# Performance work log

Measured on AMD Instinct MI355X. Metric: run time of the kernel, lower is better.

The kernel has to match this reference:

```python
import jax, jax.numpy as jnp
import numpy as np

D, H, KVH, HD, FF = 768, 12, 4, 64, 2048
N_REP = H // KVH
EPS = 1e-6


def rmsnorm(x, w):
    # Faithful to source: norm = ||x|| * n^{-1/2}; eps added to norm (not inside sqrt)
    norm = jnp.sqrt(jnp.sum(x * x, axis=-1, keepdims=True)) * (x.shape[-1] ** -0.5)
    return w * x / (norm + EPS)


def rope_tables(seq_len, head_dim, base=10000.0):
    inv_freq = 1.0 / (base ** (np.arange(0, head_dim, 2, dtype=np.float32) / head_dim))
    t = np.arange(seq_len, dtype=np.float32)
    freqs = np.einsum('i,j->ij', t, inv_freq)  # [S, HD/2]
    emb = np.concatenate([freqs, freqs], axis=-1)  # [S, HD]
    return jnp.asarray(np.cos(emb)), jnp.asarray(np.sin(emb))


def rotate_half(x):
    h = x.shape[-1] // 2
    return jnp.concatenate([-x[..., h:], x[..., :h]], axis=-1)


def setup_inputs() -> dict:
    key = jax.random.key(0)
    ks = jax.random.split(key, 9)
    s = 0.02
    return {
        'x': jax.random.normal(ks[0], (2, 2048, D), jnp.float32),
        'Wq': jax.random.normal(ks[1], (H * HD, D), jnp.float32) * s,
        'Wk': jax.random.normal(ks[2], (KVH * HD, D), jnp.float32) * s,
        'Wv': jax.random.normal(ks[3], (KVH * HD, D), jnp.float32) * s,
        'Wo': jax.random.normal(ks[4], (D, H * HD), jnp.float32) * s,
        'Wgate': jax.random.normal(ks[5], (FF, D), jnp.float32) * s,
        'Wup': jax.random.normal(ks[6], (FF, D), jnp.float32) * s,
        'Wdown': jax.random.normal(ks[7], (D, FF), jnp.float32) * s,
        'g1': jnp.ones((D,), jnp.float32),
        'g2': jnp.ones((D,), jnp.float32),
    }


def reference(x, Wq, Wk, Wv, Wo, Wgate, Wup, Wdown, g1, g2):
    B, S, _ = x.shape
    # ---- attention sublayer (pre-norm) ----
    xn = rmsnorm(x, g1)
    q = (xn @ Wq.T).reshape(B, S, H, HD).transpose(0, 2, 1, 3)      # [B,H,S,HD]
    k = (xn @ Wk.T).reshape(B, S, KVH, HD).transpose(0, 2, 1, 3)    # [B,KVH,S,HD]
    v = (xn @ Wv.T).reshape(B, S, KVH, HD).transpose(0, 2, 1, 3)
    cos, sin = rope_tables(S, HD)                                   # [S,HD]
    q = q * cos + rotate_half(q) * sin
    k = k * cos + rotate_half(k) * sin
    # repeat kv heads to match q heads
    k = jnp.repeat(k, N_REP, axis=1)                                # [B,H,S,HD]
    v = jnp.repeat(v, N_REP, axis=1)
    scores = jnp.einsum('bhqd,bhkd->bhqk', q, k) / jnp.sqrt(jnp.float32(HD))
    causal = jnp.tril(jnp.ones((S, S), bool))
    scores = jnp.where(causal, scores, jnp.finfo(scores.dtype).min)
    attn = jax.nn.softmax(scores, axis=-1)
    out = jnp.einsum('bhqk,bhkd->bhqd', attn, v)                    # [B,H,S,HD]
    out = out.transpose(0, 2, 1, 3).reshape(B, S, H * HD) @ Wo.T
    x = x + out
    # ---- SwiGLU FFN sublayer (pre-norm) ----
    xn2 = rmsnorm(x, g2)
    ff = (jax.nn.silu(xn2 @ Wgate.T) * (xn2 @ Wup.T)) @ Wdown.T
    return x + ff
```

## Files before the change

### kernel.cpp

```cpp
#include <hip/hip_runtime.h>
#include <hip/hip_bf16.h>
#include <math.h>

typedef __bf16 bf16;
typedef __attribute__((ext_vector_type(8))) __bf16 bf16x8;
typedef __attribute__((ext_vector_type(4))) __bf16 bf16x4;
typedef __attribute__((ext_vector_type(4))) float f32x4;

#define MFMA16(a,b,c) __builtin_amdgcn_mfma_f32_16x16x32_bf16(a,b,c,0,0,0)

#define BATCH 2
#define SEQ   2048
#define DMODEL 768
#define NH    12
#define NKV   4
#define NREP  3
#define HD    64
#define FFDIM 2048
#define ROWS  (BATCH*SEQ)

#define QSCALE 0.18033688011112042f
#define LOG2E  1.4426950408889634f

#define WB(N) asm volatile("s_waitcnt vmcnt(" #N ")\n\ts_barrier" ::: "memory")
#define BAR() asm volatile("s_barrier" ::: "memory")

__device__ __forceinline__ void gl2lds16(const bf16* g, bf16* l) {
  __builtin_amdgcn_global_load_lds(
      (const __attribute__((address_space(1))) void*)g,
      (__attribute__((address_space(3))) void*)l, 16, 0, 0);
}

struct Cvt7 { const float* s[7]; bf16* d[7]; int n[7]; };
__global__ __launch_bounds__(256) void cvt_all_kernel(Cvt7 c) {
  int seg = blockIdx.y;
  const float* __restrict__ src = c.s[seg];
  bf16* __restrict__ dst = c.d[seg];
  int n = c.n[seg];
  int stride = gridDim.x * 256;
  for (int i = blockIdx.x * 256 + threadIdx.x; i < n; i += stride)
    dst[i] = (bf16)src[i];
}

__global__ __launch_bounds__(256) void rope_tab_kernel(float* __restrict__ tab) {
  int id = blockIdx.x * 256 + threadIdx.x;
  int j = id >> 11, s = id & 2047;
  float inv = expf(-(float)j * (9.210340371976184f / 32.0f));
  float ang = (float)s * inv;
  tab[id] = cosf(ang);
  tab[65536 + id] = sinf(ang);
}

__global__ __launch_bounds__(192) void rmsnorm_kernel(const float* __restrict__ x,
    const float* __restrict__ g, bf16* __restrict__ out) {
  int row = blockIdx.x;
  const float* xr = x + (size_t)row * DMODEL;
  int t = threadIdx.x;
  f32x4 v = *(const f32x4*)(xr + t * 4);
  float ss = v[0] * v[0] + v[1] * v[1] + v[2] * v[2] + v[3] * v[3];
  #pragma unroll
  for (int off = 32; off; off >>= 1) ss += __shfl_xor(ss, off, 64);
  __shared__ float red[3];
  if ((t & 63) == 0) red[t >> 6] = ss;
  __syncthreads();
  float total = red[0] + red[1] + red[2];
  float norm = sqrtf(total) * 0.03608439182435161f;
  float sc = 1.0f / (norm + 1e-6f);
  f32x4 gv = *(const f32x4*)(g + t * 4);
  bf16x4 o;
  #pragma unroll
  for (int i = 0; i < 4; ++i) o[i] = (bf16)(gv[i] * v[i] * sc);
  *(bf16x4*)(out + (size_t)row * DMODEL + t * 4) = o;
}

__global__ __launch_bounds__(256) void gemm_pipe64_kernel(const bf16* __restrict__ A,
    const bf16* __restrict__ B, float* __restrict__ C, const float* __restrict__ R,
    int N, int K) {
  __shared__ __align__(16) bf16 At[4][64 * 32];
  __shared__ __align__(16) bf16 Bt[4][64 * 32];
  int t = threadIdx.x, lane = t & 63, wave = t >> 6;
  int l15 = lane & 15, lq = lane >> 4;
  int wrow = (wave >> 1) * 32, wcol = (wave & 1) * 32;
  int row0 = blockIdx.y * 64, col0 = blockIdx.x * 64;
  const bf16* Ag = A + (size_t)(row0 + (t >> 2)) * K + (t & 3) * 8;
  const bf16* Bg = B + (size_t)(col0 + (t >> 2)) * K + (t & 3) * 8;
  const int NS = K / 32;

  #pragma unroll
  for (int s = 0; s < 4; ++s) {
    int ks = s * 32;
    gl2lds16(Ag + ks, At[s] + t * 8);
    gl2lds16(Bg + ks, Bt[s] + t * 8);
  }

  f32x4 zero = {0.f, 0.f, 0.f, 0.f};
  f32x4 acc[2][2];
  #pragma unroll
  for (int m = 0; m < 2; ++m)
    #pragma unroll
    for (int n = 0; n < 2; ++n) acc[m][n] = zero;

  #define GP_COMPUTE(slot) do {                                              \
    const bf16* at = At[slot]; const bf16* bt = Bt[slot];                    \
    bf16x8 af[2], bfr[2];                                                    \
    _Pragma("unroll")                                                        \
    for (int m = 0; m < 2; ++m)                                              \
      af[m] = *(const bf16x8*)(at + (wrow + m * 16 + l15) * 32 + lq * 8);    \
    _Pragma("unroll")                                                        \
    for (int n = 0; n < 2; ++n)                                              \
      bfr[n] = *(const bf16x8*)(bt + (wcol + n * 16 + l15) * 32 + lq * 8);   \
    _Pragma("unroll")                                                        \
    for (int m = 0; m < 2; ++m)                                              \
      _Pragma("unroll")                                                      \
      for (int n = 0; n < 2; ++n)                                            \
        acc[m][n] = MFMA16(af[m], bfr[n], acc[m][n]);                        \
  } while (0)

  for (int k = 0; k < NS - 3; ++k) {
    WB(6);
    GP_COMPUTE(k & 3);
    BAR();
    if (k <= NS - 5) {
      int ks = (k + 4) * 32;
      gl2lds16(Ag + ks, At[k & 3] + t * 8);
      gl2lds16(Bg + ks, Bt[k & 3] + t * 8);
    }
  }
  for (int k = NS - 3; k < NS; ++k) {
    WB(0);
    GP_COMPUTE(k & 3);
  }
  #undef GP_COMPUTE

  #pragma unroll
  for (int m = 0; m < 2; ++m)
    #pragma unroll
    for (int n = 0; n < 2; ++n)
      #pragma unroll
      for (int r = 0; r < 4; ++r) {
        size_t idx = (size_t)(row0 + wrow + m * 16 + lq * 4 + r) * N
                   + (col0 + wcol + n * 16 + l15);
        C[idx] = acc[m][n][r] + R[idx];
      }
}

__global__ __launch_bounds__(256) void gemm_qkv_kernel(const bf16* __restrict__ A,
    const bf16* __restrict__ Wcat, const float* __restrict__ tab,
    bf16* __restrict__ Qh, bf16* __restrict__ Kh, bf16* __restrict__ Vt) {
  __shared__ __align__(16) bf16 At[4][64 * 32];
  __shared__ __align__(16) bf16 Bt[4][128 * 32];
  const int K = DMODEL;
  int t = threadIdx.x, lane = t & 63, wave = t >> 6;
  int l15 = lane & 15, lq = lane >> 4;
  int wrow = (wave >> 1) * 32, wcol = (wave & 1) * 64;
  int row0 = blockIdx.y * 64, col0 = blockIdx.x * 128;
  const bf16* Ag  = A + (size_t)(row0 + (t >> 2)) * K + (t & 3) * 8;
  const bf16* Bg0 = Wcat + (size_t)(col0 + (t >> 2)) * K + (t & 3) * 8;
  const bf16* Bg1 = Bg0 + (size_t)64 * K;
  const int NS = K / 32;

  #pragma unroll
  for (int s = 0; s < 4; ++s) {
    int ks = s * 32;
    gl2lds16(Ag + ks,  At[s] + t * 8);
    gl2lds16(Bg0 + ks, Bt[s] + t * 8);
    gl2lds16(Bg1 + ks, Bt[s] + 2048 + t * 8);
  }

  f32x4 zero = {0.f, 0.f, 0.f, 0.f};
  f32x4 acc[2][4];
  #pragma unroll
  for (int m = 0; m < 2; ++m)
    #pragma unroll
    for (int n = 0; n < 4; ++n) acc[m][n] = zero;

  #define QK_COMPUTE(slot) do {                                              \
    const bf16* at = At[slot]; const bf16* bt = Bt[slot];                    \
    bf16x8 af[2], bfr[4];                                                    \
    _Pragma("unroll")                                                        \
    for (int m = 0; m < 2; ++m)                                              \
      af[m] = *(const bf16x8*)(at + (wrow + m * 16 + l15) * 32 + lq * 8);    \
    _Pragma("unroll")                                                        \
    for (int n = 0; n < 4; ++n)                                              \
      bfr[n] = *(const bf16x8*)(bt + (wcol + n * 16 + l15) * 32 + lq * 8);   \
    _Pragma("unroll")                                                        \
    for (int m = 0; m < 2; ++m)                                              \
      _Pragma("unroll")                                                      \
      for (int n = 0; n < 4; ++n)                                            \
        acc[m][n] = MFMA16(af[m], bfr[n], acc[m][n]);                        \
  } while (0)

  for (int k = 0; k < NS - 3; ++k) {
    WB(9);
    QK_COMPUTE(k & 3);
    BAR();
    if (k <= NS - 5) {
      int ks = (k + 4) * 32;
      gl2lds16(Ag + ks,  At[k & 3] + t * 8);
      gl2lds16(Bg0 + ks, Bt[k & 3] + t * 8);
      gl2lds16(Bg1 + ks, Bt[k & 3] + 2048 + t * 8);
    }
  }
  for (int k = NS - 3; k < NS; ++k) {
    WB(0);
    QK_COMPUTE(k & 3);
  }
  #undef QK_COMPUTE

  int b = row0 >> 11;
  int s0 = (row0 & 2047) + wrow + lq * 4;
  int colw = col0 + wcol;
  if (colw < 768) {
    int h = colw >> 6;
    f32x4 cv[2][2], sv[2][2];
    #pragma unroll
    for (int m = 0; m < 2; ++m)
      #pragma unroll
      for (int jh = 0; jh < 2; ++jh) {
        const float* cp = tab + (jh * 16 + l15) * 2048 + s0 + m * 16;
        cv[m][jh] = *(const f32x4*)cp;
        sv[m][jh] = *(const f32x4*)(cp + 65536);
      }
    #pragma unroll
    for (int m = 0; m < 2; ++m)
      #pragma unroll
      for (int n = 0; n < 4; ++n) {
        float sgn = (n < 2) ? -1.f : 1.f;
        #pragma unroll
        for (int r = 0; r < 4; ++r) {
          float c = cv[m][n & 1][r], si = sv[m][n & 1][r];
          float rp = (acc[m][n][r] * c + sgn * acc[m][n ^ 2][r] * si) * QSCALE;
          Qh[((size_t)(b * NH + h) * SEQ + s0 + m * 16 + r) * 64 + n * 16 + l15] = (bf16)rp;
        }
      }
  } else if (colw < 1024) {
    int kh = (colw - 768) >> 6;
    f32x4 cv[2][2], sv[2][2];
    #pragma unroll
    for (int m = 0; m < 2; ++m)
      #pragma unroll
      for (int jh = 0; jh < 2; ++jh) {
        const float* cp = tab + (jh * 16 + l15) * 2048 + s0 + m * 16;
        cv[m][jh] = *(const f32x4*)cp;
        sv[m][jh] = *(const f32x4*)(cp + 65536);
      }
    #pragma unroll
    for (int m = 0; m < 2; ++m)
      #pragma unroll
      for (int n = 0; n < 4; ++n) {
        float sgn = (n < 2) ? -1.f : 1.f;
        #pragma unroll
        for (int r = 0; r < 4; ++r) {
          float c = cv[m][n & 1][r], si = sv[m][n & 1][r];
          float rp = acc[m][n][r] * c + sgn * acc[m][n ^ 2][r] * si;
          Kh[((size_t)(b * NKV + kh) * SEQ + s0 + m * 16 + r) * 64 + n * 16 + l15] = (bf16)rp;
        }
      }
  } else {
    int vh = (colw - 1024) >> 6;
    #pragma unroll
    for (int m = 0; m < 2; ++m)
      #pragma unroll
      for (int n = 0; n < 4; ++n) {
        bf16x4 pv;
        #pragma unroll
        for (int r = 0; r < 4; ++r) pv[r] = (bf16)acc[m][n][r];
        *(bf16x4*)(Vt + ((size_t)(b * NKV + vh) * 64 + n * 16 + l15) * SEQ + s0 + m * 16) = pv;
      }
  }
}

__global__ __launch_bounds__(256) void gemm_gu_kernel(const bf16* __restrict__ A,
    const bf16* __restrict__ Wg, const bf16* __restrict__ Wu, bf16* __restrict__ H) {
  __shared__ __align__(16) bf16 At[3][128 * 32];
  __shared__ __align__(16) bf16 Bgt[3][64 * 32];
  __shared__ __align__(16) bf16 But[3][64 * 32];
  const int K = DMODEL;
  int t = threadIdx.x, lane = t & 63, wave = t >> 6;
  int l15 = lane & 15, lq = lane >> 4;
  int wrow = (wave >> 1) * 64, wcol = (wave & 1) * 32;
  int row0 = blockIdx.y * 128, col0 = blockIdx.x * 64;
  const bf16* Ag0 = A + (size_t)(row0 + (t >> 2)) * K + (t & 3) * 8;
  const bf16* Ag1 = Ag0 + (size_t)64 * K;
  const bf16* Gg  = Wg + (size_t)(col0 + (t >> 2)) * K + (t & 3) * 8;
  const bf16* Ug  = Wu + (size_t)(col0 + (t >> 2)) * K + (t & 3) * 8;
  const int NS = K / 32;

  #pragma unroll
  for (int s = 0; s < 3; ++s) {
    int ks = s * 32;
    gl2lds16(Ag0 + ks, At[s] + t * 8);
    gl2lds16(Ag1 + ks, At[s] + 2048 + t * 8);
    gl2lds16(Gg + ks,  Bgt[s] + t * 8);
    gl2lds16(Ug + ks,  But[s] + t * 8);
  }

  f32x4 zero = {0.f, 0.f, 0.f, 0.f};
  f32x4 ag[4][2], au[4][2];
  #pragma unroll
  for (int m = 0; m < 4; ++m)
    #pragma unroll
    for (int n = 0; n < 2; ++n) { ag[m][n] = zero; au[m][n] = zero; }

  #define GU_COMPUTE(slot) do {                                              \
    const bf16* at = At[slot];                                               \
    const bf16* bgt = Bgt[slot]; const bf16* but = But[slot];                \
    bf16x8 af[4], bg[2], bu[2];                                              \
    _Pragma("unroll")                                                        \
    for (int m = 0; m < 4; ++m)                                              \
      af[m] = *(const bf16x8*)(at + (wrow + m * 16 + l15) * 32 + lq * 8);    \
    _Pragma("unroll")                                                        \
    for (int n = 0; n < 2; ++n) {                                            \
      bg[n] = *(const bf16x8*)(bgt + (wcol + n * 16 + l15) * 32 + lq * 8);   \
      bu[n] = *(const bf16x8*)(but + (wcol + n * 16 + l15) * 32 + lq * 8);   \
    }                                                                        \
    _Pragma("unroll")                                                        \
    for (int m = 0; m < 4; ++m)                                              \
      _Pragma("unroll")                                                      \
      for (int n = 0; n < 2; ++n) {                                          \
        ag[m][n] = MFMA16(af[m], bg[n], ag[m][n]);                           \
        au[m][n] = MFMA16(af[m], bu[n], au[m][n]);                           \
      }                                                                      \
  } while (0)

  int slot = 0;
  for (int k = 0; k < NS - 2; ++k) {
    WB(8);
    GU_COMPUTE(slot);
    BAR();
    if (k <= NS - 4) {
      int ks = (k + 3) * 32;
      gl2lds16(Ag0 + ks, At[slot] + t * 8);
      gl2lds16(Ag1 + ks, At[slot] + 2048 + t * 8);
      gl2lds16(Gg + ks,  Bgt[slot] + t * 8);
      gl2lds16(Ug + ks,  But[slot] + t * 8);
    }
    slot = (slot == 2) ? 0 : slot + 1;
  }
  for (int k = NS - 2; k < NS; ++k) {
    WB(0);
    GU_COMPUTE(slot);
    slot = (slot == 2) ? 0 : slot + 1;
  }
  #undef GU_COMPUTE

  #pragma unroll
  for (int m = 0; m < 4; ++m)
    #pragma unroll
    for (int n = 0; n < 2; ++n)
      #pragma unroll
      for (int r = 0; r < 4; ++r) {
        int row = row0 + wrow + m * 16 + lq * 4 + r;
        int col = col0 + wcol + n * 16 + l15;
        float g = ag[m][n][r], u = au[m][n][r];
        float sg = g / (1.f + __builtin_amdgcn_exp2f(-g * LOG2E));
        H[(size_t)row * FFDIM + col] = (bf16)(sg * u);
      }
}

__global__ __launch_bounds__(256) void attn_kernel(const bf16* __restrict__ Qh,
    const bf16* __restrict__ Kh, const bf16* __restrict__ Vt, bf16* __restrict__ out) {
  __shared__ __align__(16) bf16 Kl0[2][64 * 32];
  __shared__ __align__(16) bf16 Kl1[2][64 * 32];
  __shared__ __align__(16) bf16 Vl0[2][64 * 32];
  __shared__ __align__(16) bf16 Vl1[2][64 * 32];
  __shared__ __align__(16) bf16 P[4][16 * 80];

  int idx = blockIdx.x;
  int qt = 31 - (idx / 24);
  int bh = idx % 24;
  int q0blk = qt * 64;
  int b = bh / NH, h = bh % NH;
  int kvh = h / NREP;
  int t = threadIdx.x;
  int lane = t & 63, wave = t >> 6;
  int l15 = lane & 15, lq = lane >> 4;
  int qw = q0blk + wave * 16;
  const bf16* Qb = Qh + (size_t)(b * NH + h) * SEQ * 64;
  const bf16* Kb = Kh + (size_t)(b * NKV + kvh) * SEQ * 64;
  const bf16* Vb = Vt + (size_t)(b * NKV + kvh) * 64 * SEQ;

  bf16x8 bq0 = *(const bf16x8*)(Qb + (size_t)(qw + l15) * 64 + lq * 8);
  bf16x8 bq1 = *(const bf16x8*)(Qb + (size_t)(qw + l15) * 64 + 32 + lq * 8);

  const bf16* Kg = Kb + (size_t)(t >> 2) * 64 + (t & 3) * 8;
  const bf16* Vg = Vb + (size_t)(t >> 2) * SEQ + (t & 3) * 8;
  bf16* Pw = P[wave];
  int Pwq = l15 * 80, lq8 = lq * 8, lq4 = lq * 4;
  const int NS = qt + 1;

  #pragma unroll
  for (int s = 0; s < 2; ++s) {
    int ks = (s < NS ? s : NS - 1) * 64;
    gl2lds16(Kg + (size_t)ks * 64,      Kl0[s] + t * 8);
    gl2lds16(Kg + (size_t)ks * 64 + 32, Kl1[s] + t * 8);
    gl2lds16(Vg + ks,                   Vl0[s] + t * 8);
    gl2lds16(Vg + ks + 32,              Vl1[s] + t * 8);
  }

  f32x4 zero = {0.f, 0.f, 0.f, 0.f};
  f32x4 o[4];
  o[0] = zero; o[1] = zero; o[2] = zero; o[3] = zero;
  float l_r = 0.f;

  #define ATTN_STEP(kk, slot) do {                                           \
    int k0 = (kk) * 64;                                                      \
    const bf16* kl0 = Kl0[slot]; const bf16* kl1 = Kl1[slot];                \
    const bf16* vl0 = Vl0[slot]; const bf16* vl1 = Vl1[slot];                \
    f32x4 s[4];                                                              \
    _Pragma("unroll")                                                        \
    for (int c = 0; c < 4; ++c) {                                            \
      bf16x8 ak0 = *(const bf16x8*)(kl0 + (c * 16 + l15) * 32 + lq8);        \
      bf16x8 ak1 = *(const bf16x8*)(kl1 + (c * 16 + l15) * 32 + lq8);        \
      s[c] = zero;                                                           \
      s[c] = MFMA16(ak0, bq0, s[c]);                                         \
      s[c] = MFMA16(ak1, bq1, s[c]);                                         \
    }                                                                        \
    if (k0 + 63 > qw) {                                                      \
      int qmk = qw + l15 - k0 - lq4;                                         \
      _Pragma("unroll")                                                      \
      for (int c = 0; c < 4; ++c)                                            \
        _Pragma("unroll")                                                    \
        for (int r = 0; r < 4; ++r)                                          \
          if (c * 16 + r > qmk) s[c][r] = -INFINITY;                         \
    }                                                                        \
    _Pragma("unroll")                                                        \
    for (int c = 0; c < 4; ++c) {                                            \
      bf16x4 pe;                                                             \
      _Pragma("unroll")                                                      \
      for (int r = 0; r < 4; ++r) {                                          \
        float e = __builtin_amdgcn_exp2f(s[c][r]);                           \
        l_r += e;                                                            \
        pe[r] = (bf16)e;                                                     \
      }                                                                      \
      *(bf16x4*)(Pw + Pwq + c * 16 + lq4) = pe;                              \
    }                                                                        \
    bf16x8 bp0 = *(const bf16x8*)(Pw + Pwq + lq8);                           \
    bf16x8 bp1 = *(const bf16x8*)(Pw + Pwq + 32 + lq8);                      \
    _Pragma("unroll")                                                        \
    for (int n = 0; n < 4; ++n) {                                            \
      bf16x8 av0 = *(const bf16x8*)(vl0 + (n * 16 + l15) * 32 + lq8);        \
      bf16x8 av1 = *(const bf16x8*)(vl1 + (n * 16 + l15) * 32 + lq8);        \
      o[n] = MFMA16(av0, bp0, o[n]);                                         \
      o[n] = MFMA16(av1, bp1, o[n]);                                         \
    }                                                                        \
  } while (0)

  for (int k = 0; k < NS - 1; ++k) {
    WB(4);
    ATTN_STEP(k, k & 1);
    BAR();
    if (k <= NS - 3) {
      int ks = (k + 2) * 64;
      gl2lds16(Kg + (size_t)ks * 64,      Kl0[k & 1] + t * 8);
      gl2lds16(Kg + (size_t)ks * 64 + 32, Kl1[k & 1] + t * 8);
      gl2lds16(Vg + ks,                   Vl0[k & 1] + t * 8);
      gl2lds16(Vg + ks + 32,              Vl1[k & 1] + t * 8);
    }
  }
  {
    WB(0);
    ATTN_STEP(NS - 1, (NS - 1) & 1);
  }
  #undef ATTN_STEP

  float lt = l_r;
  lt += __shfl_xor(lt, 16, 64);
  lt += __shfl_xor(lt, 32, 64);
  float inv = 1.f / lt;
  int q = qw + l15;
  bf16* orow = out + (size_t)(b * SEQ + q) * DMODEL + h * 64;
  #pragma unroll
  for (int n = 0; n < 4; ++n) {
    bf16x4 po;
    #pragma unroll
    for (int r = 0; r < 4; ++r) po[r] = (bf16)(o[n][r] * inv);
    *(bf16x4*)(orow + n * 16 + lq4) = po;
  }
}

extern "C" void kernel_launch(void* const* d_in, const int* in_sizes, int n_in,
                              void* d_out, int out_size, void* d_ws, size_t ws_size,
                              hipStream_t stream) {
  const float* x     = (const float*)d_in[0];
  const float* Wq    = (const float*)d_in[1];
  const float* Wk    = (const float*)d_in[2];
  const float* Wv    = (const float*)d_in[3];
  const float* Wo    = (const float*)d_in[4];
  const float* Wgate = (const float*)d_in[5];
  const float* Wup   = (const float*)d_in[6];
  const float* Wdown = (const float*)d_in[7];
  const float* g1    = (const float*)d_in[8];
  const float* g2    = (const float*)d_in[9];
  float* out = (float*)d_out;

  char* ws = (char*)d_ws;
  size_t off = 0;
  auto alloc = [&](size_t bytes) { size_t o = off; off += (bytes + 255) & ~(size_t)255; return o; };
  size_t o_tab  = alloc((size_t)2 * 32 * 2048 * 4);
  size_t o_x1   = alloc((size_t)4096 * 768 * 4);
  size_t o_xn   = alloc((size_t)4096 * 768 * 2);
  size_t o_Qh   = alloc((size_t)2 * 12 * 2048 * 64 * 2);
  size_t o_Kh   = alloc((size_t)2 * 4 * 2048 * 64 * 2);
  size_t o_Vt   = alloc((size_t)2 * 4 * 64 * 2048 * 2);
  size_t o_ao   = alloc((size_t)4096 * 768 * 2);
  size_t o_H    = alloc((size_t)4096 * 2048 * 2);
  size_t o_Wcat = alloc((size_t)1280 * 768 * 2);
  size_t o_Wo   = alloc((size_t)768 * 768 * 2);
  size_t o_Wgu  = alloc((size_t)4096 * 768 * 2);
  size_t o_Wdn  = alloc((size_t)768 * 2048 * 2);
  if (ws_size < off) return;

  float* tab  = (float*)(ws + o_tab);
  float* fx1  = (float*)(ws + o_x1);
  bf16* bxn   = (bf16*)(ws + o_xn);
  bf16* bQh   = (bf16*)(ws + o_Qh);
  bf16* bKh   = (bf16*)(ws + o_Kh);
  bf16* bVt   = (bf16*)(ws + o_Vt);
  bf16* bao   = (bf16*)(ws + o_ao);
  bf16* bH    = (bf16*)(ws + o_H);
  bf16* bWcat = (bf16*)(ws + o_Wcat);
  bf16* bWo   = (bf16*)(ws + o_Wo);
  bf16* bWgu  = (bf16*)(ws + o_Wgu);
  bf16* bWdn  = (bf16*)(ws + o_Wdn);

  rope_tab_kernel<<<256, 256, 0, stream>>>(tab);

  Cvt7 c;
  c.s[0] = Wq;    c.d[0] = bWcat;              c.n[0] = 768 * 768;
  c.s[1] = Wk;    c.d[1] = bWcat + 768 * 768;  c.n[1] = 256 * 768;
  c.s[2] = Wv;    c.d[2] = bWcat + 1024 * 768; c.n[2] = 256 * 768;
  c.s[3] = Wo;    c.d[3] = bWo;                c.n[3] = 768 * 768;
  c.s[4] = Wgate; c.d[4] = bWgu;               c.n[4] = 2048 * 768;
  c.s[5] = Wup;   c.d[5] = bWgu + 2048 * 768;  c.n[5] = 2048 * 768;
  c.s[6] = Wdown; c.d[6] = bWdn;               c.n[6] = 768 * 2048;
  cvt_all_kernel<<<dim3(256, 7), 256, 0, stream>>>(c);

  rmsnorm_kernel<<<4096, 192, 0, stream>>>(x, g1, bxn);
  gemm_qkv_kernel<<<dim3(10, 64), 256, 0, stream>>>(bxn, bWcat, tab, bQh, bKh, bVt);
  attn_kernel<<<dim3(768), 256, 0, stream>>>(bQh, bKh, bVt, bao);
  gemm_pipe64_kernel<<<dim3(12, 64), 256, 0, stream>>>(bao, bWo, fx1, x, 768, 768);

  rmsnorm_kernel<<<4096, 192, 0, stream>>>(fx1, g2, bxn);
  gemm_gu_kernel<<<dim3(32, 32), 256, 0, stream>>>(bxn, bWgu, bWgu + 2048 * 768, bH);
  gemm_pipe64_kernel<<<dim3(12, 64), 256, 0, stream>>>(bH, bWdn, out, fx1, 768, 2048);
}
```

Baseline: 258.6 us.

## Swizzle LDS tiles, split-K output GEMMs across two wave groups, remap blocks

Applies an XOR swizzle to the global-to-LDS column offsets and matching LDS read offsets in the QKV, gate/up and output GEMMs to reduce LDS bank conflicts. The output-projection and down-projection GEMM becomes a 512-thread kernel where two 256-thread groups each handle half of K with a 3-stage pipeline and reduce through LDS before the residual add. A block-index remap groups tiles for better L2 reuse. This adds an LDS reduction and extra barriers, and the larger blocks may lower occupancy.

```diff
diff --git a/kernel.cpp b/kernel.cpp
--- a/kernel.cpp
+++ b/kernel.cpp
@@ -31,6 +31,9 @@
       (__attribute__((address_space(3))) void*)l, 16, 0, 0);
 }
 
+#define SRC_SWZ(tt)  ((((tt) & 3) ^ (((tt) >> 3) & 3)) * 8)
+#define RD_SWZ(l15,lq) (((lq) ^ (((l15) >> 1) & 3)) * 8)
+
 struct Cvt7 { const float* s[7]; bf16* d[7]; int n[7]; };
 __global__ __launch_bounds__(256) void cvt_all_kernel(Cvt7 c) {
   int seg = blockIdx.y;
@@ -73,24 +76,34 @@
   *(bf16x4*)(out + (size_t)row * DMODEL + t * 4) = o;
 }
 
-__global__ __launch_bounds__(256) void gemm_pipe64_kernel(const bf16* __restrict__ A,
+__global__ __launch_bounds__(512, 6) void gemm_out_kernel(const bf16* __restrict__ A,
     const bf16* __restrict__ B, float* __restrict__ C, const float* __restrict__ R,
     int N, int K) {
-  __shared__ __align__(16) bf16 At[4][64 * 32];
-  __shared__ __align__(16) bf16 Bt[4][64 * 32];
-  int t = threadIdx.x, lane = t & 63, wave = t >> 6;
+  __shared__ __align__(16) bf16 At[2][3][64 * 32];
+  __shared__ __align__(16) bf16 Bt[2][3][64 * 32];
+  int t = threadIdx.x;
+  int g = t >> 8;
+  int tt = t & 255;
+  int lane = t & 63;
+  int w = (t >> 6) & 3;
   int l15 = lane & 15, lq = lane >> 4;
-  int wrow = (wave >> 1) * 32, wcol = (wave & 1) * 32;
-  int row0 = blockIdx.y * 64, col0 = blockIdx.x * 64;
-  const bf16* Ag = A + (size_t)(row0 + (t >> 2)) * K + (t & 3) * 8;
-  const bf16* Bg = B + (size_t)(col0 + (t >> 2)) * K + (t & 3) * 8;
-  const int NS = K / 32;
-
-  #pragma unroll
-  for (int s = 0; s < 4; ++s) {
-    int ks = s * 32;
-    gl2lds16(Ag + ks, At[s] + t * 8);
-    gl2lds16(Bg + ks, Bt[s] + t * 8);
+  int wrow = (w >> 1) * 32, wcol = (w & 1) * 32;
+  int sw = RD_SWZ(l15, lq);
+
+  int flat = blockIdx.y * 12 + blockIdx.x;
+  int f2 = (flat & 7) * 96 + (flat >> 3);
+  int col0 = (f2 % 12) * 64, row0 = (f2 / 12) * 64;
+
+  const int KH = K >> 1;
+  const int NS = KH / 32;
+  int scol = SRC_SWZ(tt);
+  const bf16* Ag = A + (size_t)(row0 + (tt >> 2)) * K + g * KH + scol;
+  const bf16* Bg = B + (size_t)(col0 + (tt >> 2)) * K + g * KH + scol;
+
+  #pragma unroll
+  for (int s = 0; s < 3; ++s) {
+    gl2lds16(Ag + s * 32, At[g][s] + tt * 8);
+    gl2lds16(Bg + s * 32, Bt[g][s] + tt * 8);
   }
 
   f32x4 zero = {0.f, 0.f, 0.f, 0.f};
@@ -100,48 +113,66 @@
     #pragma unroll
     for (int n = 0; n < 2; ++n) acc[m][n] = zero;
 
-  #define GP_COMPUTE(slot) do {                                              \
-    const bf16* at = At[slot]; const bf16* bt = Bt[slot];                    \
-    bf16x8 af[2], bfr[2];                                                    \
+  #define OG_COMPUTE(slot) do {                                              \
+    const bf16* at = At[g][slot]; const bf16* bt = Bt[g][slot];              \
+    bf16x8 af[2], bb[2];                                                     \
     _Pragma("unroll")                                                        \
     for (int m = 0; m < 2; ++m)                                              \
-      af[m] = *(const bf16x8*)(at + (wrow + m * 16 + l15) * 32 + lq * 8);    \
+      af[m] = *(const bf16x8*)(at + (wrow + m * 16 + l15) * 32 + sw);        \
     _Pragma("unroll")                                                        \
     for (int n = 0; n < 2; ++n)                                              \
-      bfr[n] = *(const bf16x8*)(bt + (wcol + n * 16 + l15) * 32 + lq * 8);   \
+      bb[n] = *(const bf16x8*)(bt + (wcol + n * 16 + l15) * 32 + sw);        \
     _Pragma("unroll")                                                        \
     for (int m = 0; m < 2; ++m)                                              \
       _Pragma("unroll")                                                      \
       for (int n = 0; n < 2; ++n)                                            \
-        acc[m][n] = MFMA16(af[m], bfr[n], acc[m][n]);                        \
+        acc[m][n] = MFMA16(af[m], bb[n], acc[m][n]);                         \
   } while (0)
 
-  for (int k = 0; k < NS - 3; ++k) {
-    WB(6);
-    GP_COMPUTE(k & 3);
+  int slot = 0;
+  for (int k = 0; k < NS - 2; ++k) {
+    WB(4);
+    OG_COMPUTE(slot);
     BAR();
-    if (k <= NS - 5) {
-      int ks = (k + 4) * 32;
-      gl2lds16(Ag + ks, At[k & 3] + t * 8);
-      gl2lds16(Bg + ks, Bt[k & 3] + t * 8);
+    if (k <= NS - 4) {
+      int ks = (k + 3) * 32;
+      gl2lds16(Ag + ks, At[g][slot] + tt * 8);
+      gl2lds16(Bg + ks, Bt[g][slot] + tt * 8);
     }
-  }
-  for (int k = NS - 3; k < NS; ++k) {
+    slot = (slot == 2) ? 0 : slot + 1;
+  }
+  for (int k = NS - 2; k < NS; ++k) {
     WB(0);
-    GP_COMPUTE(k & 3);
-  }
-  #undef GP_COMPUTE
-
-  #pragma unroll
-  for (int m = 0; m < 2; ++m)
-    #pragma unroll
-    for (int n = 0; n < 2; ++n)
-      #pragma unroll
-      for (int r = 0; r < 4; ++r) {
-        size_t idx = (size_t)(row0 + wrow + m * 16 + lq * 4 + r) * N
-                   + (col0 + wcol + n * 16 + l15);
-        C[idx] = acc[m][n][r] + R[idx];
-      }
+    OG_COMPUTE(slot);
+    slot = (slot == 2) ? 0 : slot + 1;
+  }
+  #undef OG_COMPUTE
+
+  __syncthreads();
+  float* Cl = (float*)&At[0][0][0];
+  if (g == 1) {
+    #pragma unroll
+    for (int m = 0; m < 2; ++m)
+      #pragma unroll
+      for (int n = 0; n < 2; ++n)
+        #pragma unroll
+        for (int r = 0; r < 4; ++r)
+          Cl[(wrow + m * 16 + lq * 4 + r) * 64 + wcol + n * 16 + l15] = acc[m][n][r];
+  }
+  __syncthreads();
+  if (g == 0) {
+    #pragma unroll
+    for (int m = 0; m < 2; ++m)
+      #pragma unroll
+      for (int n = 0; n < 2; ++n)
+        #pragma unroll
+        for (int r = 0; r < 4; ++r) {
+          int row = wrow + m * 16 + lq * 4 + r;
+          int col = wcol + n * 16 + l15;
+          size_t idx = (size_t)(row0 + row) * N + col0 + col;
+          C[idx] = acc[m][n][r] + Cl[row * 64 + col] + R[idx];
+        }
+  }
 }
 
 __global__ __launch_bounds__(256) void gemm_qkv_kernel(const bf16* __restrict__ A,
@@ -153,9 +184,11 @@
   int t = threadIdx.x, lane = t & 63, wave = t >> 6;
   int l15 = lane & 15, lq = lane >> 4;
   int wrow = (wave >> 1) * 32, wcol = (wave & 1) * 64;
+  int sw = RD_SWZ(l15, lq);
   int row0 = blockIdx.y * 64, col0 = blockIdx.x * 128;
-  const bf16* Ag  = A + (size_t)(row0 + (t >> 2)) * K + (t & 3) * 8;
-  const bf16* Bg0 = Wcat + (size_t)(col0 + (t >> 2)) * K + (t & 3) * 8;
+  int scol = SRC_SWZ(t);
+  const bf16* Ag  = A + (size_t)(row0 + (t >> 2)) * K + scol;
+  const bf16* Bg0 = Wcat + (size_t)(col0 + (t >> 2)) * K + scol;
   const bf16* Bg1 = Bg0 + (size_t)64 * K;
   const int NS = K / 32;
 
@@ -179,10 +212,10 @@
     bf16x8 af[2], bfr[4];                                                    \
     _Pragma("unroll")                                                        \
     for (int m = 0; m < 2; ++m)                                              \
-      af[m] = *(const bf16x8*)(at + (wrow + m * 16 + l15) * 32 + lq * 8);    \
+      af[m] = *(const bf16x8*)(at + (wrow + m * 16 + l15) * 32 + sw);        \
     _Pragma("unroll")                                                        \
     for (int n = 0; n < 4; ++n)                                              \
-      bfr[n] = *(const bf16x8*)(bt + (wcol + n * 16 + l15) * 32 + lq * 8);   \
+      bfr[n] = *(const bf16x8*)(bt + (wcol + n * 16 + l15) * 32 + sw);       \
     _Pragma("unroll")                                                        \
     for (int m = 0; m < 2; ++m)                                              \
       _Pragma("unroll")                                                      \
@@ -279,11 +312,13 @@
   int t = threadIdx.x, lane = t & 63, wave = t >> 6;
   int l15 = lane & 15, lq = lane >> 4;
   int wrow = (wave >> 1) * 64, wcol = (wave & 1) * 32;
+  int sw = RD_SWZ(l15, lq);
   int row0 = blockIdx.y * 128, col0 = blockIdx.x * 64;
-  const bf16* Ag0 = A + (size_t)(row0 + (t >> 2)) * K + (t & 3) * 8;
+  int scol = SRC_SWZ(t);
+  const bf16* Ag0 = A + (size_t)(row0 + (t >> 2)) * K + scol;
   const bf16* Ag1 = Ag0 + (size_t)64 * K;
-  const bf16* Gg  = Wg + (size_t)(col0 + (t >> 2)) * K + (t & 3) * 8;
-  const bf16* Ug  = Wu + (size_t)(col0 + (t >> 2)) * K + (t & 3) * 8;
+  const bf16* Gg  = Wg + (size_t)(col0 + (t >> 2)) * K + scol;
+  const bf16* Ug  = Wu + (size_t)(col0 + (t >> 2)) * K + scol;
   const int NS = K / 32;
 
   #pragma unroll
@@ -308,11 +343,11 @@
     bf16x8 af[4], bg[2], bu[2];                                              \
     _Pragma("unroll")                                                        \
     for (int m = 0; m < 4; ++m)                                              \
-      af[m] = *(const bf16x8*)(at + (wrow + m * 16 + l15) * 32 + lq * 8);    \
+      af[m] = *(const bf16x8*)(at + (wrow + m * 16 + l15) * 32 + sw);        \
     _Pragma("unroll")                                                        \
     for (int n = 0; n < 2; ++n) {                                            \
-      bg[n] = *(const bf16x8*)(bgt + (wcol + n * 16 + l15) * 32 + lq * 8);   \
-      bu[n] = *(const bf16x8*)(but + (wcol + n * 16 + l15) * 32 + lq * 8);   \
+      bg[n] = *(const bf16x8*)(bgt + (wcol + n * 16 + l15) * 32 + sw);       \
+      bu[n] = *(const bf16x8*)(but + (wcol + n * 16 + l15) * 32 + sw);       \
     }                                                                        \
     _Pragma("unroll")                                                        \
     for (int m = 0; m < 4; ++m)                                              \
@@ -539,9 +574,9 @@
   rmsnorm_kernel<<<4096, 192, 0, stream>>>(x, g1, bxn);
   gemm_qkv_kernel<<<dim3(10, 64), 256, 0, stream>>>(bxn, bWcat, tab, bQh, bKh, bVt);
   attn_kernel<<<dim3(768), 256, 0, stream>>>(bQh, bKh, bVt, bao);
-  gemm_pipe64_kernel<<<dim3(12, 64), 256, 0, stream>>>(bao, bWo, fx1, x, 768, 768);
+  gemm_out_kernel<<<dim3(12, 64), 512, 0, stream>>>(bao, bWo, fx1, x, 768, 768);
 
   rmsnorm_kernel<<<4096, 192, 0, stream>>>(fx1, g2, bxn);
   gemm_gu_kernel<<<dim3(32, 32), 256, 0, stream>>>(bxn, bWgu, bWgu + 2048 * 768, bH);
-  gemm_pipe64_kernel<<<dim3(12, 64), 256, 0, stream>>>(bH, bWdn, out, fx1, 768, 2048);
-}
+  gemm_out_kernel<<<dim3(12, 64), 512, 0, stream>>>(bH, bWdn, out, fx1, 768, 2048);
+}
```

Result: faster. 245.8 us (-5.0%).
